# Optimization experiments

Measured on AMD Instinct MI355X. Metric: run time of the kernel, lower is better.

Reference implementation:

```python
import jax, jax.numpy as jnp
import numpy as np

NUM_STATES = 64
HIDDEN = 32
NUM_ACTIONS = 3
SEQ_LEN = 512
BATCH = 2048


def setup_inputs() -> dict:
    key = jax.random.key(0)
    ks = jax.random.split(key, 7)
    s_ih = 1.0 / np.sqrt(HIDDEN)
    x = jax.random.normal(ks[0], (SEQ_LEN, BATCH, NUM_STATES), dtype=jnp.float32)
    # PyTorch LSTM params: gate order [i, f, g, o], each block of size HIDDEN
    W_ih = jax.random.uniform(ks[1], (4 * HIDDEN, NUM_STATES), minval=-s_ih, maxval=s_ih, dtype=jnp.float32)
    W_hh = jax.random.uniform(ks[2], (4 * HIDDEN, HIDDEN), minval=-s_ih, maxval=s_ih, dtype=jnp.float32)
    b_ih = jax.random.uniform(ks[3], (4 * HIDDEN,), minval=-s_ih, maxval=s_ih, dtype=jnp.float32)
    b_hh = jax.random.uniform(ks[4], (4 * HIDDEN,), minval=-s_ih, maxval=s_ih, dtype=jnp.float32)
    s_d = 1.0 / np.sqrt(HIDDEN)
    W_d = jax.random.uniform(ks[5], (NUM_ACTIONS, HIDDEN), minval=-s_d, maxval=s_d, dtype=jnp.float32)
    b_d = jax.random.uniform(ks[6], (NUM_ACTIONS,), minval=-s_d, maxval=s_d, dtype=jnp.float32)
    return {"x": x, "W_ih": W_ih, "W_hh": W_hh, "b_ih": b_ih, "b_hh": b_hh, "W_d": W_d, "b_d": b_d}


def _lstm_last_hidden(x, W_ih, W_hh, b_ih, b_hh):
    # x: [T, B, F] time-major, as in nn.LSTM(batch_first=False)
    B = x.shape[1]
    H = W_hh.shape[1]
    # Precompute input projections for all timesteps in one GEMM: [T, B, 4H]
    x_proj = jnp.einsum('tbf,gf->tbg', x, W_ih) + (b_ih + b_hh)

    def step(carry, xp_t):
        h, c = carry
        gates = xp_t + h @ W_hh.T  # [B, 4H]
        i, f, g, o = jnp.split(gates, 4, axis=-1)
        i = jax.nn.sigmoid(i)
        f = jax.nn.sigmoid(f)
        g = jnp.tanh(g)
        o = jax.nn.sigmoid(o)
        c = f * c + i * g
        h = o * jnp.tanh(c)
        return (h, c), None

    h0 = jnp.zeros((B, H), dtype=x.dtype)
    c0 = jnp.zeros((B, H), dtype=x.dtype)
    (h_T, _), _ = jax.lax.scan(step, (h0, c0), x_proj)
    return h_T  # [B, H] == lstm output at last timestep (x[-1,:,:])


def reference(x, W_ih, W_hh, b_ih, b_hh, W_d, b_d):
    h_T = _lstm_last_hidden(x, W_ih, W_hh, b_ih, b_hh)
    h = jax.nn.relu(h_T)
    return h @ W_d.T + b_d  # [B, num_actions]
```

## Files before the change

### kernel.cpp

```cpp
#include <hip/hip_runtime.h>

typedef __bf16 bf16_t;
typedef __bf16 bf16x8 __attribute__((ext_vector_type(8)));
typedef float  f32x4  __attribute__((ext_vector_type(4)));

#define T_STEPS 512
#define BATCH   2048
#define NS      64
#define FSTR    36

#define K_SIG  (-1.4426950408889634f)
#define K_TANH ( 2.8853900817779268f)

#define MFMA(A, B, C) __builtin_amdgcn_mfma_f32_16x16x32_bf16((A), (B), (C), 0, 0, 0)

__global__ __launch_bounds__(64, 1) __attribute__((amdgpu_waves_per_eu(1, 1)))
void lstm_policy_kernel(const float* __restrict__ x,
                        const float* __restrict__ W_ih,
                        const float* __restrict__ W_hh,
                        const float* __restrict__ b_ih,
                        const float* __restrict__ b_hh,
                        const float* __restrict__ W_d,
                        const float* __restrict__ b_d,
                        float* __restrict__ out)
{
  __shared__ float hf[16 * FSTR];

  const int lane = threadIdx.x;
  const int m    = lane & 15;
  const int q    = lane >> 4;
  const int row0 = blockIdx.x << 4;

  bf16x8 a_ih[4][2][2], a_hh[4][2];
  f32x4  bias[4][2];
  #pragma unroll
  for (int G = 0; G < 4; ++G) {
    const float k = (G == 2) ? K_TANH : K_SIG;
    #pragma unroll
    for (int U = 0; U < 2; ++U) {
      const int wrow = (G << 5) + (U << 4) + m;
      const float* pih = W_ih + wrow * 64;
      const float* phh = W_hh + (wrow << 5);
      #pragma unroll
      for (int j = 0; j < 8; ++j) {
        a_ih[G][U][0][j] = (bf16_t)(k * pih[(q << 3) + j]);
        a_ih[G][U][1][j] = (bf16_t)(k * pih[32 + (q << 3) + j]);
        const int us = (j < 4) ? ((q << 2) + j) : (16 + (q << 2) + (j - 4));
        a_hh[G][U][j] = (bf16_t)(k * phh[us]);
      }
      #pragma unroll
      for (int r = 0; r < 4; ++r) {
        const int u = (G << 5) + (U << 4) + (q << 2) + r;
        bias[G][U][r] = (b_ih[u] + b_hh[u]) * k;
      }
    }
  }

  const size_t xstep = (size_t)BATCH * NS;
  const float* xb = x + (size_t)row0 * NS;
  const int    lo = m * NS + (q << 3);

  f32x4 xf[4][4];
  {
    const float* p1 = xb + 1 * xstep + lo;
    const float* p2 = xb + 2 * xstep + lo;
    const float* p3 = xb + 3 * xstep + lo;
    const float* p4 = xb + 4 * xstep + lo;
    xf[1][0]=*(const f32x4*)(p1); xf[1][1]=*(const f32x4*)(p1+4); xf[1][2]=*(const f32x4*)(p1+32); xf[1][3]=*(const f32x4*)(p1+36);
    xf[2][0]=*(const f32x4*)(p2); xf[2][1]=*(const f32x4*)(p2+4); xf[2][2]=*(const f32x4*)(p2+32); xf[2][3]=*(const f32x4*)(p2+36);
    xf[3][0]=*(const f32x4*)(p3); xf[3][1]=*(const f32x4*)(p3+4); xf[3][2]=*(const f32x4*)(p3+32); xf[3][3]=*(const f32x4*)(p3+36);
    xf[0][0]=*(const f32x4*)(p4); xf[0][1]=*(const f32x4*)(p4+4); xf[0][2]=*(const f32x4*)(p4+32); xf[0][3]=*(const f32x4*)(p4+36);
  }

  f32x4 acc[4][2];
  {
    const float* p0 = xb + lo;
    f32x4 x0a = *(const f32x4*)(p0),      x0b = *(const f32x4*)(p0 + 4);
    f32x4 x0c = *(const f32x4*)(p0 + 32), x0d = *(const f32x4*)(p0 + 36);
    bf16x8 xA, xB;
    #pragma unroll
    for (int j = 0; j < 4; ++j) {
      xA[j] = (bf16_t)x0a[j]; xA[4+j] = (bf16_t)x0b[j];
      xB[j] = (bf16_t)x0c[j]; xB[4+j] = (bf16_t)x0d[j];
    }
    #pragma unroll
    for (int G = 0; G < 4; ++G)
      #pragma unroll
      for (int U = 0; U < 2; ++U) {
        acc[G][U] = MFMA(a_ih[G][U][0], xA, bias[G][U]);
        acc[G][U] = MFMA(a_ih[G][U][1], xB, acc[G][U]);
      }
  }

  float cst[2][4] = {{0,0,0,0},{0,0,0,0}};
  bf16x8 hB = {};

  #define STEP(P)                                                                     \
  do {                                                                                \
    const int tt = t + (P);                                                           \
    f32x4 gr[4][2];                                                                   \
    _Pragma("unroll")                                                                 \
    for (int G = 0; G < 4; ++G)                                                       \
      _Pragma("unroll")                                                               \
      for (int U = 0; U < 2; ++U)                                                     \
        gr[G][U] = MFMA(a_hh[G][U], hB, acc[G][U]);                                   \
                      \
    {                                                                                 \
      const int ns = ((P) + 1) & 3;                                                   \
      bf16x8 xA, xB;                                                                  \
      _Pragma("unroll")                                                               \
      for (int j = 0; j < 4; ++j) {                                                   \
        xA[j] = (bf16_t)xf[ns][0][j]; xA[4+j] = (bf16_t)xf[ns][1][j];                 \
        xB[j] = (bf16_t)xf[ns][2][j]; xB[4+j] = (bf16_t)xf[ns][3][j];                 \
      }                                                                               \
      _Pragma("unroll")                                                               \
      for (int G = 0; G < 4; ++G)                                                     \
        _Pragma("unroll")                                                             \
        for (int U = 0; U < 2; ++U) {                                                 \
          acc[G][U] = MFMA(a_ih[G][U][0], xA, bias[G][U]);                            \
          acc[G][U] = MFMA(a_ih[G][U][1], xB, acc[G][U]);                             \
        }                                                                             \
      int tp = tt + 5; if (tp > T_STEPS - 1) tp = T_STEPS - 1;                        \
      const float* pf = xb + (size_t)tp * xstep + lo;                                 \
      xf[ns][0] = *(const f32x4*)(pf);                                                \
      xf[ns][1] = *(const f32x4*)(pf + 4);                                            \
      xf[ns][2] = *(const f32x4*)(pf + 32);                                           \
      xf[ns][3] = *(const f32x4*)(pf + 36);                                           \
    }                                                                                 \
                  \
    _Pragma("unroll")                                                                 \
    for (int U = 0; U < 2; ++U)                                                       \
      _Pragma("unroll")                                                               \
      for (int r = 0; r < 4; ++r) {                                                   \
        const float iv = __builtin_amdgcn_rcpf(1.0f + __builtin_amdgcn_exp2f(gr[0][U][r])); \
        const float fv = __builtin_amdgcn_rcpf(1.0f + __builtin_amdgcn_exp2f(gr[1][U][r])); \
        const float rg = __builtin_amdgcn_rcpf(1.0f + __builtin_amdgcn_exp2f(gr[2][U][r])); \
        const float ov = __builtin_amdgcn_rcpf(1.0f + __builtin_amdgcn_exp2f(gr[3][U][r])); \
        const float gs = __builtin_fmaf(-2.0f * K_TANH, rg, K_TANH);   \
        const float cn = __builtin_fmaf(fv, cst[U][r], iv * gs);        \
        cst[U][r] = cn;                                                               \
        const float rh  = __builtin_amdgcn_rcpf(1.0f + __builtin_amdgcn_exp2f(cn));   \
        const float ov2 = ov + ov;                                                    \
        const float h   = __builtin_fmaf(-ov2, rh, ov);                \
        hB[(U << 2) + r] = (bf16_t)h;                                                 \
        if (tt == T_STEPS - 1) hf[m * FSTR + (U << 4) + (q << 2) + r] = fmaxf(h, 0.0f); \
      }                                                                               \
  } while (0)

  #pragma unroll 1
  for (int t = 0; t < T_STEPS; t += 4) {
    STEP(0);
    STEP(1);
    STEP(2);
    STEP(3);
  }
  #undef STEP

  __syncthreads();

  if (lane < 48) {
    const int r = lane / 3;
    const int a = lane - r * 3;
    float s = b_d[a];
    #pragma unroll
    for (int u = 0; u < 32; ++u)
      s += hf[r * FSTR + u] * W_d[a * 32 + u];
    out[(size_t)(row0 + r) * 3 + a] = s;
  }
}

extern "C" void kernel_launch(void* const* d_in, const int* in_sizes, int n_in,
                              void* d_out, int out_size, void* d_ws, size_t ws_size,
                              hipStream_t stream) {
  const float* x    = (const float*)d_in[0];
  const float* W_ih = (const float*)d_in[1];
  const float* W_hh = (const float*)d_in[2];
  const float* b_ih = (const float*)d_in[3];
  const float* b_hh = (const float*)d_in[4];
  const float* W_d  = (const float*)d_in[5];
  const float* b_d  = (const float*)d_in[6];
  float* out = (float*)d_out;

  dim3 grid(BATCH / 16);
  dim3 block(64);
  hipLaunchKernelGGL(lstm_policy_kernel, grid, block, 0, stream,
                     x, W_ih, W_hh, b_ih, b_hh, W_d, b_d, out);
}
```

Before: 604.1 us.

## Split LSTM cell work across four waves with LDS hidden-state exchange

Each block now runs four waves instead of one. Each wave owns half of the hidden units and half of the accumulator rows, so per-step MFMA count and transcendental cell math per lane shrink. The new hidden state is packed to bf16, exchanged through a double-buffered LDS array with one barrier per step, and reassembled into the MFMA operand. This adds a barrier and LDS round trip to every serial step, and the input-projection work is duplicated between waves that share the same unit half.

```diff
diff --git a/kernel.cpp b/kernel.cpp
--- a/kernel.cpp
+++ b/kernel.cpp
@@ -3,6 +3,7 @@
 typedef __bf16 bf16_t;
 typedef __bf16 bf16x8 __attribute__((ext_vector_type(8)));
 typedef float  f32x4  __attribute__((ext_vector_type(4)));
+typedef unsigned int u32x4 __attribute__((ext_vector_type(4)));
 
 #define T_STEPS 512
 #define BATCH   2048
@@ -13,8 +14,13 @@
 #define K_TANH ( 2.8853900817779268f)
 
 #define MFMA(A, B, C) __builtin_amdgcn_mfma_f32_16x16x32_bf16((A), (B), (C), 0, 0, 0)
-
-__global__ __launch_bounds__(64, 1) __attribute__((amdgpu_waves_per_eu(1, 1)))
+#define RCPE(xv) __builtin_amdgcn_rcpf(1.0f + __builtin_amdgcn_exp2f(xv))
+
+__device__ __forceinline__ void barrier_lgkm() {
+  asm volatile("s_waitcnt lgkmcnt(0)\n\ts_barrier" ::: "memory");
+}
+
+__global__ __launch_bounds__(256, 1) __attribute__((amdgpu_waves_per_eu(1, 1)))
 void lstm_policy_kernel(const float* __restrict__ x,
                         const float* __restrict__ W_ih,
                         const float* __restrict__ W_hh,
@@ -24,35 +30,37 @@
                         const float* __restrict__ b_d,
                         float* __restrict__ out)
 {
+  __shared__ unsigned int hlds[2][4][64];
   __shared__ float hf[16 * FSTR];
 
-  const int lane = threadIdx.x;
+  const int tid  = threadIdx.x;
+  const int wv   = tid >> 6;
+  const int lane = tid & 63;
   const int m    = lane & 15;
   const int q    = lane >> 4;
+  const int U    = wv >> 1;
+  const int rsel = wv & 1;
   const int row0 = blockIdx.x << 4;
 
-  bf16x8 a_ih[4][2][2], a_hh[4][2];
-  f32x4  bias[4][2];
+  bf16x8 a_ih[4][2], a_hh[4];
+  f32x4  bias[4];
   #pragma unroll
   for (int G = 0; G < 4; ++G) {
     const float k = (G == 2) ? K_TANH : K_SIG;
-    #pragma unroll
-    for (int U = 0; U < 2; ++U) {
-      const int wrow = (G << 5) + (U << 4) + m;
-      const float* pih = W_ih + wrow * 64;
-      const float* phh = W_hh + (wrow << 5);
-      #pragma unroll
-      for (int j = 0; j < 8; ++j) {
-        a_ih[G][U][0][j] = (bf16_t)(k * pih[(q << 3) + j]);
-        a_ih[G][U][1][j] = (bf16_t)(k * pih[32 + (q << 3) + j]);
-        const int us = (j < 4) ? ((q << 2) + j) : (16 + (q << 2) + (j - 4));
-        a_hh[G][U][j] = (bf16_t)(k * phh[us]);
-      }
-      #pragma unroll
-      for (int r = 0; r < 4; ++r) {
-        const int u = (G << 5) + (U << 4) + (q << 2) + r;
-        bias[G][U][r] = (b_ih[u] + b_hh[u]) * k;
-      }
+    const int wrow = (G << 5) + (U << 4) + m;
+    const float* pih = W_ih + wrow * 64;
+    const float* phh = W_hh + (wrow << 5);
+    #pragma unroll
+    for (int j = 0; j < 8; ++j) {
+      a_ih[G][0][j] = (bf16_t)(k * pih[(q << 3) + j]);
+      a_ih[G][1][j] = (bf16_t)(k * pih[32 + (q << 3) + j]);
+      const int us = (j < 4) ? ((q << 2) + j) : (16 + (q << 2) + (j - 4));
+      a_hh[G][j] = (bf16_t)(k * phh[us]);
+    }
+    #pragma unroll
+    for (int r = 0; r < 4; ++r) {
+      const int u = (G << 5) + (U << 4) + (q << 2) + r;
+      bias[G][r] = (b_ih[u] + b_hh[u]) * k;
     }
   }
 
@@ -72,7 +80,7 @@
     xf[0][0]=*(const f32x4*)(p4); xf[0][1]=*(const f32x4*)(p4+4); xf[0][2]=*(const f32x4*)(p4+32); xf[0][3]=*(const f32x4*)(p4+36);
   }
 
-  f32x4 acc[4][2];
+  f32x4 acc[4];
   {
     const float* p0 = xb + lo;
     f32x4 x0a = *(const f32x4*)(p0),      x0b = *(const f32x4*)(p0 + 4);
@@ -84,67 +92,76 @@
       xB[j] = (bf16_t)x0c[j]; xB[4+j] = (bf16_t)x0d[j];
     }
     #pragma unroll
-    for (int G = 0; G < 4; ++G)
-      #pragma unroll
-      for (int U = 0; U < 2; ++U) {
-        acc[G][U] = MFMA(a_ih[G][U][0], xA, bias[G][U]);
-        acc[G][U] = MFMA(a_ih[G][U][1], xB, acc[G][U]);
-      }
-  }
-
-  float cst[2][4] = {{0,0,0,0},{0,0,0,0}};
+    for (int G = 0; G < 4; ++G) {
+      acc[G] = MFMA(a_ih[G][0], xA, bias[G]);
+      acc[G] = MFMA(a_ih[G][1], xB, acc[G]);
+    }
+  }
+
+  float cst[2] = {0.0f, 0.0f};
   bf16x8 hB = {};
 
-  #define STEP(P)                                                                     \
-  do {                                                                                \
-    const int tt = t + (P);                                                           \
-    f32x4 gr[4][2];                                                                   \
-    _Pragma("unroll")                                                                 \
-    for (int G = 0; G < 4; ++G)                                                       \
-      _Pragma("unroll")                                                               \
-      for (int U = 0; U < 2; ++U)                                                     \
-        gr[G][U] = MFMA(a_hh[G][U], hB, acc[G][U]);                                   \
-                      \
-    {                                                                                 \
-      const int ns = ((P) + 1) & 3;                                                   \
-      bf16x8 xA, xB;                                                                  \
-      _Pragma("unroll")                                                               \
-      for (int j = 0; j < 4; ++j) {                                                   \
-        xA[j] = (bf16_t)xf[ns][0][j]; xA[4+j] = (bf16_t)xf[ns][1][j];                 \
-        xB[j] = (bf16_t)xf[ns][2][j]; xB[4+j] = (bf16_t)xf[ns][3][j];                 \
-      }                                                                               \
-      _Pragma("unroll")                                                               \
-      for (int G = 0; G < 4; ++G)                                                     \
-        _Pragma("unroll")                                                             \
-        for (int U = 0; U < 2; ++U) {                                                 \
-          acc[G][U] = MFMA(a_ih[G][U][0], xA, bias[G][U]);                            \
-          acc[G][U] = MFMA(a_ih[G][U][1], xB, acc[G][U]);                             \
-        }                                                                             \
-      int tp = tt + 5; if (tp > T_STEPS - 1) tp = T_STEPS - 1;                        \
-      const float* pf = xb + (size_t)tp * xstep + lo;                                 \
-      xf[ns][0] = *(const f32x4*)(pf);                                                \
-      xf[ns][1] = *(const f32x4*)(pf + 4);                                            \
-      xf[ns][2] = *(const f32x4*)(pf + 32);                                           \
-      xf[ns][3] = *(const f32x4*)(pf + 36);                                           \
-    }                                                                                 \
-                  \
-    _Pragma("unroll")                                                                 \
-    for (int U = 0; U < 2; ++U)                                                       \
-      _Pragma("unroll")                                                               \
-      for (int r = 0; r < 4; ++r) {                                                   \
-        const float iv = __builtin_amdgcn_rcpf(1.0f + __builtin_amdgcn_exp2f(gr[0][U][r])); \
-        const float fv = __builtin_amdgcn_rcpf(1.0f + __builtin_amdgcn_exp2f(gr[1][U][r])); \
-        const float rg = __builtin_amdgcn_rcpf(1.0f + __builtin_amdgcn_exp2f(gr[2][U][r])); \
-        const float ov = __builtin_amdgcn_rcpf(1.0f + __builtin_amdgcn_exp2f(gr[3][U][r])); \
-        const float gs = __builtin_fmaf(-2.0f * K_TANH, rg, K_TANH);   \
-        const float cn = __builtin_fmaf(fv, cst[U][r], iv * gs);        \
-        cst[U][r] = cn;                                                               \
-        const float rh  = __builtin_amdgcn_rcpf(1.0f + __builtin_amdgcn_exp2f(cn));   \
-        const float ov2 = ov + ov;                                                    \
-        const float h   = __builtin_fmaf(-ov2, rh, ov);                \
-        hB[(U << 2) + r] = (bf16_t)h;                                                 \
-        if (tt == T_STEPS - 1) hf[m * FSTR + (U << 4) + (q << 2) + r] = fmaxf(h, 0.0f); \
-      }                                                                               \
+  #define CELL(RR, E, HOUT)                                                         \
+    {                                                                               \
+      const float iv = RCPE(gr[0][RR]);                                             \
+      const float fv = RCPE(gr[1][RR]);                                             \
+      const float rg = RCPE(gr[2][RR]);                                             \
+      const float ov = RCPE(gr[3][RR]);                                             \
+      const float gs = __builtin_fmaf(-2.0f * K_TANH, rg, K_TANH);   \
+      const float cn = __builtin_fmaf(fv, cst[E], iv * gs);           \
+      cst[E] = cn;                                                                  \
+      const float rh  = RCPE(cn);                                                   \
+      const float ov2 = ov + ov;                                                    \
+      HOUT = __builtin_fmaf(-ov2, rh, ov);                           \
+      if (tt == T_STEPS - 1) hf[m * FSTR + (U << 4) + (q << 2) + RR] = fmaxf(HOUT, 0.0f); \
+    }
+
+  #define STEP(P)                                                                   \
+  do {                                                                              \
+    const int tt  = t + (P);                                                        \
+    const int par = (P) & 1;                                                        \
+    f32x4 gr[4];                                                                    \
+    _Pragma("unroll")                                                               \
+    for (int G = 0; G < 4; ++G)                                                     \
+      gr[G] = MFMA(a_hh[G], hB, acc[G]);                                            \
+    float h0, h1;                                                                   \
+    if (rsel == 0) { CELL(0, 0, h0) CELL(1, 1, h1) }                                \
+    else           { CELL(2, 0, h0) CELL(3, 1, h1) }                                \
+    {                                                                               \
+      const unsigned int s0 = __builtin_bit_cast(unsigned short, (bf16_t)h0);       \
+      const unsigned int s1 = __builtin_bit_cast(unsigned short, (bf16_t)h1);       \
+      hlds[par][wv][lane] = s0 | (s1 << 16);                                        \
+    }                                                                               \
+    barrier_lgkm();                                                                 \
+    const unsigned int w0 = hlds[par][0][lane];                                     \
+    const unsigned int w1 = hlds[par][1][lane];                                     \
+    const unsigned int w2 = hlds[par][2][lane];                                     \
+    const unsigned int w3 = hlds[par][3][lane];                                     \
+                \
+    {                                                                               \
+      const int ns = ((P) + 1) & 3;                                                 \
+      bf16x8 xA, xB;                                                                \
+      _Pragma("unroll")                                                             \
+      for (int j = 0; j < 4; ++j) {                                                 \
+        xA[j] = (bf16_t)xf[ns][0][j]; xA[4+j] = (bf16_t)xf[ns][1][j];               \
+        xB[j] = (bf16_t)xf[ns][2][j]; xB[4+j] = (bf16_t)xf[ns][3][j];               \
+      }                                                                             \
+      _Pragma("unroll")                                                             \
+      for (int G = 0; G < 4; ++G) {                                                 \
+        acc[G] = MFMA(a_ih[G][0], xA, bias[G]);                                     \
+        acc[G] = MFMA(a_ih[G][1], xB, acc[G]);                                      \
+      }                                                                             \
+      int tp = tt + 5; if (tp > T_STEPS - 1) tp = T_STEPS - 1;                      \
+      const float* pf = xb + (size_t)tp * xstep + lo;                               \
+      xf[ns][0] = *(const f32x4*)(pf);                                              \
+      xf[ns][1] = *(const f32x4*)(pf + 4);                                          \
+      xf[ns][2] = *(const f32x4*)(pf + 32);                                         \
+      xf[ns][3] = *(const f32x4*)(pf + 36);                                         \
+    }                                                                               \
+    {                                                                               \
+      u32x4 hw; hw[0] = w0; hw[1] = w1; hw[2] = w2; hw[3] = w3;                     \
+      hB = __builtin_bit_cast(bf16x8, hw);                                          \
+    }                                                                               \
   } while (0)
 
   #pragma unroll 1
@@ -155,12 +172,13 @@
     STEP(3);
   }
   #undef STEP
+  #undef CELL
 
   __syncthreads();
 
-  if (lane < 48) {
-    const int r = lane / 3;
-    const int a = lane - r * 3;
+  if (tid < 48) {
+    const int r = tid / 3;
+    const int a = tid - r * 3;
     float s = b_d[a];
     #pragma unroll
     for (int u = 0; u < 32; ++u)
@@ -182,7 +200,7 @@
   float* out = (float*)d_out;
 
   dim3 grid(BATCH / 16);
-  dim3 block(64);
+  dim3 block(256);
   hipLaunchKernelGGL(lstm_policy_kernel, grid, block, 0, stream,
                      x, W_ih, W_hh, b_ih, b_hh, W_d, b_d, out);
 }
```

Result: faster. 526.6 us (-12.8%).
